# Kernel tuning notes

Measured on AMD Instinct MI355X. Metric: run time of the kernel, lower is better.

The kernel has to match this reference:

```python
import jax, jax.numpy as jnp
import numpy as np

N_NODES = 100000
N_EDGES = 1250000
IN_NDIM = 128
OUT_NDIM = 64


def setup_inputs() -> dict:
    key = jax.random.key(0)
    ks = jax.random.split(key, 8)
    return {
        "node_feats": jax.random.normal(ks[0], (N_NODES, IN_NDIM), dtype=jnp.float32),
        "edge_d": jax.random.uniform(ks[1], (N_EDGES, 1), dtype=jnp.float32),
        "W0": jax.random.normal(ks[2], (1, 1), dtype=jnp.float32),
        "W1": jax.random.normal(ks[3], (OUT_NDIM, IN_NDIM), dtype=jnp.float32) * (IN_NDIM ** -0.5),
        "W2": jax.random.normal(ks[4], (OUT_NDIM, IN_NDIM), dtype=jnp.float32) * (IN_NDIM ** -0.5),
        "Wa": jax.random.normal(ks[5], (1, 2 * OUT_NDIM + 1), dtype=jnp.float32) * (OUT_NDIM ** -0.5),
        "src": jax.random.randint(ks[6], (N_EDGES,), 0, N_NODES, dtype=jnp.int32),
        "dst": jax.random.randint(ks[7], (N_EDGES,), 0, N_NODES, dtype=jnp.int32),
    }


def reference(node_feats, edge_d, W0, W1, W2, Wa, src, dst):
    N = node_feats.shape[0]
    # fc1 / fc2 node projections (bias-free linears)
    z = node_feats @ W1.T            # [N, out_ndim]
    z_i = node_feats @ W2.T          # [N, out_ndim]
    # fc0 edge feature projection
    t = edge_d @ W0.T                # [E, 1]
    # gather per-edge endpoint features
    z_src = z[src]                   # [E, out_ndim]
    z_dst = z[dst]                   # [E, out_ndim]
    # attention logit: leaky_relu(attn_fc([z_src, z_dst, t]))
    a = jnp.concatenate([z_src, z_dst, t], axis=1) @ Wa.T   # [E, 1]
    e = jax.nn.leaky_relu(a[:, 0], 0.01)                      # torch default slope
    # segment softmax over incoming edges of each dst node
    m = jax.ops.segment_max(e, dst, num_segments=N)          # -inf for empty segs
    ex = jnp.exp(e - m[dst])
    denom = jax.ops.segment_sum(ex, dst, num_segments=N)
    alpha = ex / denom[dst]                                   # [E]
    # weighted scatter-sum of source messages
    z_neighbor = jax.ops.segment_sum(alpha[:, None] * z_src, dst, num_segments=N)
    h = jax.nn.relu(z_i + z_neighbor)
    return h
```

## Files before the change

### kernel.cpp

```cpp
#include <hip/hip_runtime.h>

#define N_NODES 100000
#define N_EDGES 1250000
#define IN_D 128
#define OUT_D 64
#define BSHIFT 7
#define NBUCK  782
#define CAP    2560
#define EPB    4096
#define NBLK_E 306
#define NBLK_G 1563

typedef __attribute__((ext_vector_type(8))) __bf16 bf16x8;
typedef __attribute__((ext_vector_type(4))) float floatx4;

__device__ __forceinline__ float2 up2(unsigned u) {
    return make_float2(__uint_as_float(u << 16),
                       __uint_as_float(u & 0xFFFF0000u));
}

__global__ __launch_bounds__(256) void fusedA_kernel(
    const float* __restrict__ x, const float* __restrict__ W1,
    const float* __restrict__ W2, const float* __restrict__ W0,
    const float* __restrict__ Wa,
    const int* __restrict__ dst, const int* __restrict__ src,
    const float* __restrict__ edge_d,
    int* __restrict__ gcur, uint2* __restrict__ payA,
    unsigned short* __restrict__ zb, unsigned short* __restrict__ zib,
    float* __restrict__ s1, float* __restrict__ s2)
{
    __shared__ __bf16 sB[16384];
    __shared__ float  sWa[128];
    __shared__ int    h[NBUCK];
    __shared__ int    lcur[NBUCK];

    const int t = threadIdx.x;

    if (blockIdx.x < NBLK_E) {
        const float tc = W0[0] * Wa[2 * OUT_D];
        for (int i = t; i < NBUCK; i += 256) h[i] = 0;
        __syncthreads();
        const int base = blockIdx.x * EPB;
        int4 d4[4]; bool val[4];
        #pragma unroll
        for (int k = 0; k < 4; ++k) {
            int i = base + k * 1024 + t * 4;
            val[k] = (i < N_EDGES);
            if (val[k]) {
                d4[k] = *(const int4*)(dst + i);
                atomicAdd(&h[d4[k].x >> BSHIFT], 1);
                atomicAdd(&h[d4[k].y >> BSHIFT], 1);
                atomicAdd(&h[d4[k].z >> BSHIFT], 1);
                atomicAdd(&h[d4[k].w >> BSHIFT], 1);
            }
        }
        __syncthreads();
        for (int b = t; b < NBUCK; b += 256) {
            int hc = h[b];
            int p = hc ? atomicAdd(&gcur[b], hc) : 0;
            lcur[b] = b * CAP + p;
        }
        __syncthreads();
        #define EMIT(dv, sv, ev)                                              \
            { int bk = (dv) >> BSHIFT;                                        \
              int pos = atomicAdd(&lcur[bk], 1);                              \
              if (pos < (bk + 1) * CAP)                                       \
                  payA[pos] = make_uint2((unsigned)(sv) |                     \
                                         ((unsigned)((dv) & 127) << 17),      \
                                         __float_as_uint(tc * (ev))); }
        #pragma unroll
        for (int k = 0; k < 4; ++k) {
            int i = base + k * 1024 + t * 4;
            if (val[k]) {
                int4   s4 = *(const int4*)(src + i);
                float4 e4 = *(const float4*)(edge_d + i);
                EMIT(d4[k].x, s4.x, e4.x);
                EMIT(d4[k].y, s4.y, e4.y);
                EMIT(d4[k].z, s4.z, e4.z);
                EMIT(d4[k].w, s4.w, e4.w);
            }
        }
        #undef EMIT
        return;
    }

    #pragma unroll
    for (int g = 0; g < 8; ++g) {
        int gi = t + g * 256;
        int n  = gi >> 4;
        int k8 = gi & 15;
        const float* wrow = (n < 64) ? (W1 + n * 128) : (W2 + (n - 64) * 128);
        float4 v0 = *(const float4*)(wrow + k8 * 8);
        float4 v1 = *(const float4*)(wrow + k8 * 8 + 4);
        int lane = ((k8 & 3) << 4) | (n & 15);
        int off  = (((n >> 4) * 4 + (k8 >> 2)) * 64 + lane) * 8;
        bf16x8 bb;
        bb[0] = (__bf16)v0.x; bb[1] = (__bf16)v0.y;
        bb[2] = (__bf16)v0.z; bb[3] = (__bf16)v0.w;
        bb[4] = (__bf16)v1.x; bb[5] = (__bf16)v1.y;
        bb[6] = (__bf16)v1.z; bb[7] = (__bf16)v1.w;
        *(bf16x8*)(sB + off) = bb;
    }
    if (t < 128) sWa[t] = Wa[t];
    __syncthreads();

    const int lane = t & 63;
    const int wave = t >> 6;
    const int tile = (blockIdx.x - NBLK_E) * 4 + wave;
    if (tile * 16 >= N_NODES) return;

    const int n0 = tile * 16;
    const int m  = lane & 15;
    const int kb = lane >> 4;

    floatx4 acc[8];
    #pragma unroll
    for (int q = 0; q < 8; ++q) acc[q] = (floatx4)(0.f);

    const float* xrow = x + (size_t)(n0 + m) * IN_D;

    #pragma unroll
    for (int kc = 0; kc < 4; ++kc) {
        float4 v0 = *(const float4*)(xrow + kc * 32 + kb * 8);
        float4 v1 = *(const float4*)(xrow + kc * 32 + kb * 8 + 4);
        float xs[8] = {v0.x, v0.y, v0.z, v0.w, v1.x, v1.y, v1.z, v1.w};
        bf16x8 ahi, alo;
        #pragma unroll
        for (int j = 0; j < 8; ++j) {
            __bf16 hh = (__bf16)xs[j];
            ahi[j] = hh;
            alo[j] = (__bf16)(xs[j] - (float)hh);
        }
        #pragma unroll
        for (int nt = 0; nt < 8; ++nt) {
            int off = ((nt * 4 + kc) * 64 + lane) * 8;
            bf16x8 b = *(const bf16x8*)(sB + off);
            acc[nt] = __builtin_amdgcn_mfma_f32_16x16x32_bf16(ahi, b, acc[nt], 0, 0, 0);
            acc[nt] = __builtin_amdgcn_mfma_f32_16x16x32_bf16(alo, b, acc[nt], 0, 0, 0);
        }
    }

    #pragma unroll
    for (int nt = 0; nt < 8; ++nt) {
        int col = (nt & 3) * 16 + m;
        unsigned short* dp = (nt < 4) ? zb : zib;
        #pragma unroll
        for (int reg = 0; reg < 4; ++reg) {
            int row = n0 + kb * 4 + reg;
            __bf16 hh = (__bf16)acc[nt][reg];
            dp[(size_t)row * OUT_D + col] = *(unsigned short*)&hh;
        }
    }

    #pragma unroll
    for (int reg = 0; reg < 4; ++reg) {
        float p1 = 0.f, p2 = 0.f;
        #pragma unroll
        for (int nt = 0; nt < 4; ++nt) {
            float zv = acc[nt][reg];
            p1 += zv * sWa[nt * 16 + m];
            p2 += zv * sWa[64 + nt * 16 + m];
        }
        #pragma unroll
        for (int off = 8; off > 0; off >>= 1) {
            p1 += __shfl_xor(p1, off);
            p2 += __shfl_xor(p2, off);
        }
        if (m == 0) {
            int row = n0 + kb * 4 + reg;
            s1[row] = p1;
            s2[row] = p2;
        }
    }
}

__global__ __launch_bounds__(512) void sortgather_kernel(
    const int* __restrict__ gcur, const uint2* __restrict__ payA,
    const float* __restrict__ s1, const float* __restrict__ s2,
    const unsigned short* __restrict__ zb, const unsigned short* __restrict__ zib,
    float* __restrict__ out)
{
    __shared__ uint2 sorted[CAP];
    __shared__ int   h[128];
    __shared__ int   st[128];
    __shared__ int   lc[128];
    __shared__ float s2s[128];
    __shared__ uint2 buf[16][32];

    const int b = blockIdx.x, t = threadIdx.x;
    const int n0 = b << BSHIFT;
    const int base = b * CAP;
    const int cnt = min(gcur[b], CAP);
    const int lane = t & 63;
    const int wave = t >> 6;

    if (t < 128) {
        h[t] = 0;
        int node = n0 + t;
        s2s[t] = (node < N_NODES) ? s2[node] : 0.f;
    }
    __syncthreads();

    for (int i = t; i < cnt; i += 512) {
        uint2 p = payA[base + i];
        atomicAdd(&h[(p.x >> 17) & 127], 1);
    }
    __syncthreads();

    if (wave == 0) {
        int v0 = h[lane];
        int v1 = h[lane + 64];
        int s0 = v0, s1v = v1;
        #pragma unroll
        for (int off = 1; off < 64; off <<= 1) {
            int u0 = __shfl_up(s0, off);
            int u1 = __shfl_up(s1v, off);
            if (lane >= off) { s0 += u0; s1v += u1; }
        }
        int tot0 = __shfl(s0, 63);
        s1v += tot0;
        int e0 = s0 - v0, e1 = s1v - v1;
        st[lane] = e0;      lc[lane] = e0;
        st[lane + 64] = e1; lc[lane + 64] = e1;
    }
    __syncthreads();

    for (int i = t; i < cnt; i += 512) {
        uint2 p = payA[base + i];
        int dl = (p.x >> 17) & 127;
        int pos = atomicAdd(&lc[dl], 1);
        sorted[pos] = make_uint2(p.x & 0x1FFFFu, p.y);
    }
    __syncthreads();

    const int half = lane >> 5;
    const int lh   = lane & 31;
    const int slot = wave * 2 + half;
    const int eC = lh >> 3;
    const int c  = lh & 7;

    for (int r = 0; r < 8; ++r) {
        const int ln   = slot + r * 16;
        const int node = n0 + ln;
        const int beg  = st[ln];
        const int len  = h[ln];
        const float s2d = s2s[ln];

        float den = 0.f;
        float2 a0 = make_float2(0.f, 0.f), a1 = a0, a2 = a0, a3 = a0;

        for (int o = 0; o < len; o += 32) {
            int rem = len - o;
            bool vv = lh < rem;
            uint2 p = sorted[beg + o + (vv ? lh : 0)];
            float ex = 0.f;
            if (vv) {
                float a = __uint_as_float(p.y) + s1[p.x] + s2d;
                float e = (a > 0.f) ? a : 0.01f * a;
                ex = __expf(e);
                buf[slot][lh] = make_uint2(p.x, __float_as_uint(ex));
            }
            den += ex;

            int cnt2 = min(32, rem);
            int nIt = (cnt2 + 3) >> 2;
            uint2 pe = buf[slot][(eC < cnt2) ? eC : 0];
            float exe = (eC < cnt2) ? __uint_as_float(pe.y) : 0.f;
            uint4 zv = *(const uint4*)(zb + (size_t)pe.x * OUT_D + c * 8);
            for (int g = 0; g < nIt; ++g) {
                uint2 peN; float exeN = 0.f; uint4 zvN;
                if (g + 1 < nIt) {
                    int j = (g + 1) * 4 + eC;
                    peN  = buf[slot][(j < cnt2) ? j : 0];
                    exeN = (j < cnt2) ? __uint_as_float(peN.y) : 0.f;
                    zvN  = *(const uint4*)(zb + (size_t)peN.x * OUT_D + c * 8);
                }
                float2 w0 = up2(zv.x), w1 = up2(zv.y), w2 = up2(zv.z), w3 = up2(zv.w);
                a0.x = fmaf(exe, w0.x, a0.x); a0.y = fmaf(exe, w0.y, a0.y);
                a1.x = fmaf(exe, w1.x, a1.x); a1.y = fmaf(exe, w1.y, a1.y);
                a2.x = fmaf(exe, w2.x, a2.x); a2.y = fmaf(exe, w2.y, a2.y);
                a3.x = fmaf(exe, w3.x, a3.x); a3.y = fmaf(exe, w3.y, a3.y);
                pe = peN; exe = exeN; zv = zvN;
            }
        }

        #pragma unroll
        for (int off = 16; off > 0; off >>= 1) den += __shfl_xor(den, off);
        #pragma unroll
        for (int off = 8; off <= 16; off <<= 1) {
            a0.x += __shfl_xor(a0.x, off); a0.y += __shfl_xor(a0.y, off);
            a1.x += __shfl_xor(a1.x, off); a1.y += __shfl_xor(a1.y, off);
            a2.x += __shfl_xor(a2.x, off); a2.y += __shfl_xor(a2.y, off);
            a3.x += __shfl_xor(a3.x, off); a3.y += __shfl_xor(a3.y, off);
        }

        if (lh < 8 && node < N_NODES) {
            float inv = (den > 0.f) ? 1.f / den : 0.f;
            uint4 zv = *(const uint4*)(zib + (size_t)node * OUT_D + lh * 8);
            float2 w0 = up2(zv.x), w1 = up2(zv.y), w2 = up2(zv.z), w3 = up2(zv.w);
            float4 o0, o1;
            o0.x = fmaxf(w0.x + a0.x * inv, 0.f);
            o0.y = fmaxf(w0.y + a0.y * inv, 0.f);
            o0.z = fmaxf(w1.x + a1.x * inv, 0.f);
            o0.w = fmaxf(w1.y + a1.y * inv, 0.f);
            o1.x = fmaxf(w2.x + a2.x * inv, 0.f);
            o1.y = fmaxf(w2.y + a2.y * inv, 0.f);
            o1.z = fmaxf(w3.x + a3.x * inv, 0.f);
            o1.w = fmaxf(w3.y + a3.y * inv, 0.f);
            *(float4*)(out + (size_t)node * OUT_D + lh * 8)     = o0;
            *(float4*)(out + (size_t)node * OUT_D + lh * 8 + 4) = o1;
        }
    }
}

extern "C" void kernel_launch(void* const* d_in, const int* in_sizes, int n_in,
                              void* d_out, int out_size, void* d_ws, size_t ws_size,
                              hipStream_t stream) {
    const float* node_feats = (const float*)d_in[0];
    const float* edge_d     = (const float*)d_in[1];
    const float* W0         = (const float*)d_in[2];
    const float* W1         = (const float*)d_in[3];
    const float* W2         = (const float*)d_in[4];
    const float* Wa         = (const float*)d_in[5];
    const int*   src        = (const int*)d_in[6];
    const int*   dst        = (const int*)d_in[7];
    float* out = (float*)d_out;

    char* ws = (char*)d_ws;
    uint2* payA = (uint2*)ws;    ws += (size_t)NBUCK * CAP * 8;
    unsigned short* zbuf = (unsigned short*)ws; ws += (size_t)N_NODES * OUT_D * 2;
    unsigned short* zib  = (unsigned short*)ws; ws += (size_t)N_NODES * OUT_D * 2;
    float* s1 = (float*)ws;      ws += (size_t)N_NODES * 4;
    float* s2 = (float*)ws;      ws += (size_t)N_NODES * 4;
    int*   gcur = (int*)ws;      ws += ((NBUCK + 3) & ~3) * 4;

    hipMemsetAsync(gcur, 0, NBUCK * 4, stream);

    fusedA_kernel<<<NBLK_E + NBLK_G, 256, 0, stream>>>(
        node_feats, W1, W2, W0, Wa, dst, src, edge_d,
        gcur, payA, zbuf, zib, s1, s2);

    sortgather_kernel<<<NBUCK, 512, 0, stream>>>(
        gcur, payA, s1, s2, zbuf, zib, out);
}
```

Measured before the change: 183.9 us.

## Split node GEMM blocks by output half and overlay shared memory with union

The GEMM portion of the fused kernel now launches twice as many blocks, each computing either the W1 or W2 projection for its tile. Each block holds half the weight matrix in shared memory and half the accumulators. The partition and GEMM shared buffers are overlaid in a union, which cuts LDS use per block and raises occupancy and parallelism. The cost is that each node row of x is read twice from global memory (once per half), plus the extra block-launch overhead.

```diff
diff --git a/kernel.cpp b/kernel.cpp
--- a/kernel.cpp
+++ b/kernel.cpp
@@ -9,7 +9,9 @@
 #define CAP    2560
 #define EPB    4096
 #define NBLK_E 306
-#define NBLK_G 1563
+#define NTILE  6250
+#define NBLK_H 1563
+#define NBLK_G (2*NBLK_H)
 
 typedef __attribute__((ext_vector_type(8))) __bf16 bf16x8;
 typedef __attribute__((ext_vector_type(4))) float floatx4;
@@ -29,14 +31,16 @@
     unsigned short* __restrict__ zb, unsigned short* __restrict__ zib,
     float* __restrict__ s1, float* __restrict__ s2)
 {
-    __shared__ __bf16 sB[16384];
-    __shared__ float  sWa[128];
-    __shared__ int    h[NBUCK];
-    __shared__ int    lcur[NBUCK];
+    __shared__ union U {
+        struct { int h[NBUCK]; int lcur[NBUCK]; } pa;
+        struct { alignas(16) __bf16 sB[8192]; float sWa[128]; } ge;
+    } sm;
 
     const int t = threadIdx.x;
 
     if (blockIdx.x < NBLK_E) {
+        int* h    = sm.pa.h;
+        int* lcur = sm.pa.lcur;
         const float tc = W0[0] * Wa[2 * OUT_D];
         for (int i = t; i < NBUCK; i += 256) h[i] = 0;
         __syncthreads();
@@ -84,12 +88,19 @@
         return;
     }
 
+    __bf16* sB  = sm.ge.sB;
+    float*  sWa = sm.ge.sWa;
+    const int gb   = blockIdx.x - NBLK_E;
+    const int half = gb & 1;
+    const int tg   = gb >> 1;
+
+    const float* Wh = half ? W2 : W1;
     #pragma unroll
-    for (int g = 0; g < 8; ++g) {
+    for (int g = 0; g < 4; ++g) {
         int gi = t + g * 256;
         int n  = gi >> 4;
         int k8 = gi & 15;
-        const float* wrow = (n < 64) ? (W1 + n * 128) : (W2 + (n - 64) * 128);
+        const float* wrow = Wh + n * 128;
         float4 v0 = *(const float4*)(wrow + k8 * 8);
         float4 v1 = *(const float4*)(wrow + k8 * 8 + 4);
         int lane = ((k8 & 3) << 4) | (n & 15);
@@ -106,16 +117,16 @@
 
     const int lane = t & 63;
     const int wave = t >> 6;
-    const int tile = (blockIdx.x - NBLK_E) * 4 + wave;
-    if (tile * 16 >= N_NODES) return;
+    const int tile = tg * 4 + wave;
+    if (tile >= NTILE) return;
 
     const int n0 = tile * 16;
     const int m  = lane & 15;
     const int kb = lane >> 4;
 
-    floatx4 acc[8];
+    floatx4 acc[4];
     #pragma unroll
-    for (int q = 0; q < 8; ++q) acc[q] = (floatx4)(0.f);
+    for (int q = 0; q < 4; ++q) acc[q] = (floatx4)(0.f);
 
     const float* xrow = x + (size_t)(n0 + m) * IN_D;
 
@@ -132,7 +143,7 @@
             alo[j] = (__bf16)(xs[j] - (float)hh);
         }
         #pragma unroll
-        for (int nt = 0; nt < 8; ++nt) {
+        for (int nt = 0; nt < 4; ++nt) {
             int off = ((nt * 4 + kc) * 64 + lane) * 8;
             bf16x8 b = *(const bf16x8*)(sB + off);
             acc[nt] = __builtin_amdgcn_mfma_f32_16x16x32_bf16(ahi, b, acc[nt], 0, 0, 0);
@@ -140,10 +151,10 @@
         }
     }
 
+    unsigned short* dp = half ? zib : zb;
     #pragma unroll
-    for (int nt = 0; nt < 8; ++nt) {
-        int col = (nt & 3) * 16 + m;
-        unsigned short* dp = (nt < 4) ? zb : zib;
+    for (int nt = 0; nt < 4; ++nt) {
+        int col = nt * 16 + m;
         #pragma unroll
         for (int reg = 0; reg < 4; ++reg) {
             int row = n0 + kb * 4 + reg;
@@ -152,24 +163,26 @@
         }
     }
 
-    #pragma unroll
-    for (int reg = 0; reg < 4; ++reg) {
-        float p1 = 0.f, p2 = 0.f;
-        #pragma unroll
-        for (int nt = 0; nt < 4; ++nt) {
-            float zv = acc[nt][reg];
-            p1 += zv * sWa[nt * 16 + m];
-            p2 += zv * sWa[64 + nt * 16 + m];
-        }
-        #pragma unroll
-        for (int off = 8; off > 0; off >>= 1) {
-            p1 += __shfl_xor(p1, off);
-            p2 += __shfl_xor(p2, off);
-        }
-        if (m == 0) {
-            int row = n0 + kb * 4 + reg;
-            s1[row] = p1;
-            s2[row] = p2;
+    if (half == 0) {
+        #pragma unroll
+        for (int reg = 0; reg < 4; ++reg) {
+            float p1 = 0.f, p2 = 0.f;
+            #pragma unroll
+            for (int nt = 0; nt < 4; ++nt) {
+                float zv = acc[nt][reg];
+                p1 += zv * sWa[nt * 16 + m];
+                p2 += zv * sWa[64 + nt * 16 + m];
+            }
+            #pragma unroll
+            for (int off = 8; off > 0; off >>= 1) {
+                p1 += __shfl_xor(p1, off);
+                p2 += __shfl_xor(p2, off);
+            }
+            if (m == 0) {
+                int row = n0 + kb * 4 + reg;
+                s1[row] = p1;
+                s2[row] = p2;
+            }
         }
     }
 }
```

Measured after the change: 187.2 us. Within noise of the previous version (+1.8%).

## Replace LDS bucket histogram with padded global atomics and widen blocks to 512

Applied to the files above, without the earlier changes.

The edge-binning path drops its per-block shared-memory histogram and prefix reservation. Each edge now does a global atomicAdd directly on a per-bucket counter, padded to a 16-int stride to avoid contention on the same cache line. Blocks grow to 512 threads, so each binning block covers its 4096 edges in two passes and each GEMM block handles 8 tiles. This removes two barriers and a second read of dst, but issues about 1.25M global atomics instead of roughly 782 per block, and edges within a bucket lose their locality.

```diff
diff --git a/kernel.cpp b/kernel.cpp
--- a/kernel.cpp
+++ b/kernel.cpp
@@ -7,9 +7,11 @@
 #define BSHIFT 7
 #define NBUCK  782
 #define CAP    2560
+#define GSTRIDE 16
 #define EPB    4096
 #define NBLK_E 306
-#define NBLK_G 1563
+#define NTILE  6250
+#define NBLK_W 782
 
 typedef __attribute__((ext_vector_type(8))) __bf16 bf16x8;
 typedef __attribute__((ext_vector_type(4))) float floatx4;
@@ -19,7 +21,7 @@
                        __uint_as_float(u & 0xFFFF0000u));
 }
 
-__global__ __launch_bounds__(256) void fusedA_kernel(
+__global__ __launch_bounds__(512, 8) void fusedA_kernel(
     const float* __restrict__ x, const float* __restrict__ W1,
     const float* __restrict__ W2, const float* __restrict__ W0,
     const float* __restrict__ Wa,
@@ -31,53 +33,31 @@
 {
     __shared__ __bf16 sB[16384];
     __shared__ float  sWa[128];
-    __shared__ int    h[NBUCK];
-    __shared__ int    lcur[NBUCK];
 
     const int t = threadIdx.x;
 
     if (blockIdx.x < NBLK_E) {
         const float tc = W0[0] * Wa[2 * OUT_D];
-        for (int i = t; i < NBUCK; i += 256) h[i] = 0;
-        __syncthreads();
         const int base = blockIdx.x * EPB;
-        int4 d4[4]; bool val[4];
-        #pragma unroll
-        for (int k = 0; k < 4; ++k) {
-            int i = base + k * 1024 + t * 4;
-            val[k] = (i < N_EDGES);
-            if (val[k]) {
-                d4[k] = *(const int4*)(dst + i);
-                atomicAdd(&h[d4[k].x >> BSHIFT], 1);
-                atomicAdd(&h[d4[k].y >> BSHIFT], 1);
-                atomicAdd(&h[d4[k].z >> BSHIFT], 1);
-                atomicAdd(&h[d4[k].w >> BSHIFT], 1);
-            }
-        }
-        __syncthreads();
-        for (int b = t; b < NBUCK; b += 256) {
-            int hc = h[b];
-            int p = hc ? atomicAdd(&gcur[b], hc) : 0;
-            lcur[b] = b * CAP + p;
-        }
-        __syncthreads();
         #define EMIT(dv, sv, ev)                                              \
             { int bk = (dv) >> BSHIFT;                                        \
-              int pos = atomicAdd(&lcur[bk], 1);                              \
-              if (pos < (bk + 1) * CAP)                                       \
-                  payA[pos] = make_uint2((unsigned)(sv) |                     \
-                                         ((unsigned)((dv) & 127) << 17),      \
-                                         __float_as_uint(tc * (ev))); }
-        #pragma unroll
-        for (int k = 0; k < 4; ++k) {
-            int i = base + k * 1024 + t * 4;
-            if (val[k]) {
+              int pos = atomicAdd(&gcur[bk * GSTRIDE], 1);                    \
+              if (pos < CAP)                                                  \
+                  payA[(size_t)bk * CAP + pos] =                              \
+                      make_uint2((unsigned)(sv) |                             \
+                                 ((unsigned)((dv) & 127) << 17),              \
+                                 __float_as_uint(tc * (ev))); }
+        #pragma unroll
+        for (int k0 = 0; k0 < EPB; k0 += 2048) {
+            int i = base + k0 + t * 4;
+            if (i < N_EDGES) {
+                int4   d4 = *(const int4*)(dst + i);
                 int4   s4 = *(const int4*)(src + i);
                 float4 e4 = *(const float4*)(edge_d + i);
-                EMIT(d4[k].x, s4.x, e4.x);
-                EMIT(d4[k].y, s4.y, e4.y);
-                EMIT(d4[k].z, s4.z, e4.z);
-                EMIT(d4[k].w, s4.w, e4.w);
+                EMIT(d4.x, s4.x, e4.x);
+                EMIT(d4.y, s4.y, e4.y);
+                EMIT(d4.z, s4.z, e4.z);
+                EMIT(d4.w, s4.w, e4.w);
             }
         }
         #undef EMIT
@@ -85,8 +65,8 @@
     }
 
     #pragma unroll
-    for (int g = 0; g < 8; ++g) {
-        int gi = t + g * 256;
+    for (int g = 0; g < 4; ++g) {
+        int gi = t + g * 512;
         int n  = gi >> 4;
         int k8 = gi & 15;
         const float* wrow = (n < 64) ? (W1 + n * 128) : (W2 + (n - 64) * 128);
@@ -106,8 +86,8 @@
 
     const int lane = t & 63;
     const int wave = t >> 6;
-    const int tile = (blockIdx.x - NBLK_E) * 4 + wave;
-    if (tile * 16 >= N_NODES) return;
+    const int tile = (blockIdx.x - NBLK_E) * 8 + wave;
+    if (tile >= NTILE) return;
 
     const int n0 = tile * 16;
     const int m  = lane & 15;
@@ -190,7 +170,7 @@
     const int b = blockIdx.x, t = threadIdx.x;
     const int n0 = b << BSHIFT;
     const int base = b * CAP;
-    const int cnt = min(gcur[b], CAP);
+    const int cnt = min(gcur[b * GSTRIDE], CAP);
     const int lane = t & 63;
     const int wave = t >> 6;
 
@@ -332,11 +312,11 @@
     unsigned short* zib  = (unsigned short*)ws; ws += (size_t)N_NODES * OUT_D * 2;
     float* s1 = (float*)ws;      ws += (size_t)N_NODES * 4;
     float* s2 = (float*)ws;      ws += (size_t)N_NODES * 4;
-    int*   gcur = (int*)ws;      ws += ((NBUCK + 3) & ~3) * 4;
-
-    hipMemsetAsync(gcur, 0, NBUCK * 4, stream);
-
-    fusedA_kernel<<<NBLK_E + NBLK_G, 256, 0, stream>>>(
+    int*   gcur = (int*)ws;      ws += (size_t)NBUCK * GSTRIDE * 4;
+
+    hipMemsetAsync(gcur, 0, (size_t)NBUCK * GSTRIDE * 4, stream);
+
+    fusedA_kernel<<<NBLK_E + NBLK_W, 512, 0, stream>>>(
         node_feats, W1, W2, W0, Wa, dst, src, edge_d,
         gcur, payA, zbuf, zib, s1, s2);
 
```

Result: slower. 224.3 us (+22.0%).
